# Kernel optimization log

Hardware: AMD Instinct MI355X
Metric: run time of the kernel (lower is better)

## Reference

```python
import jax, jax.numpy as jnp
import numpy as np

B_SZ, S, D_IN, D_OUT = 4, 4096, 4096, 4096
E, R = 16, 16


def setup_inputs() -> dict:
    key = jax.random.key(0)
    ks = jax.random.split(key, 6)
    x = jax.random.normal(ks[0], (B_SZ, S, D_IN), dtype=jnp.float32)
    W = jax.random.normal(ks[1], (D_OUT, D_IN), dtype=jnp.float32) * (1.0 / np.sqrt(D_IN))
    b = jax.random.normal(ks[2], (D_OUT,), dtype=jnp.float32) * 0.01
    A = jax.random.normal(ks[3], (E, R, D_IN), dtype=jnp.float32) * (1.0 / np.sqrt(D_IN))
    Bw = jax.random.normal(ks[4], (E, D_OUT, R), dtype=jnp.float32) * (1.0 / np.sqrt(R))
    probs = jax.random.uniform(ks[5], (E,), dtype=jnp.float32)
    probs = probs / jnp.sum(probs)  # router softmax-like cached probabilities
    return {"x": x, "W": W, "b": b, "A": A, "B": Bw, "probs": probs}


def reference(x, W, b, A, B, probs):
    # Base layer: out = x @ W^T + b  -> [b, s, d_out]
    out = jnp.einsum('bsd,od->bso', x, W) + b
    # LoRA mixture: sum_e probs[e] * (x @ A_e^T) @ B_e^T
    # h: [b, s, e, r] -- tiny (rank 16), then project up and weight by probs.
    h = jnp.einsum('bsd,erd->bser', x, A)
    contrib = jnp.einsum('bser,e,eor->bso', h, probs, B)
    return out + contrib
```

## Files before the change

kernel.cpp:

```cpp
#include <hip/hip_runtime.h>
#include <hip/hip_bf16.h>

typedef __bf16 bf16_t;
typedef __attribute__((ext_vector_type(8))) __bf16 bf16x8;
typedef __attribute__((ext_vector_type(4))) __bf16 bf16x4;
typedef __attribute__((ext_vector_type(4))) float f32x4;

#define GM 16384
#define GN 4096
#define GK 4096

#define GLOAD16(gp, lp)                                                        \
  __builtin_amdgcn_global_load_lds(                                            \
      (const __attribute__((address_space(1))) unsigned int*)(gp),             \
      (__attribute__((address_space(3))) unsigned int*)(lp), 16, 0, 0)

__global__ __launch_bounds__(256) void cvt_x_kernel(
    const float* __restrict__ in, bf16_t* __restrict__ outb) {
  long i = (long)blockIdx.x * blockDim.x + threadIdx.x;
  const f32x4* v = (const f32x4*)in;
  f32x4 a = v[4 * i + 0];
  f32x4 b = v[4 * i + 1];
  f32x4 c = v[4 * i + 2];
  f32x4 d = v[4 * i + 3];
  bf16x8 r0, r1;
  r0[0] = (__bf16)a[0]; r0[1] = (__bf16)a[1]; r0[2] = (__bf16)a[2]; r0[3] = (__bf16)a[3];
  r0[4] = (__bf16)b[0]; r0[5] = (__bf16)b[1]; r0[6] = (__bf16)b[2]; r0[7] = (__bf16)b[3];
  r1[0] = (__bf16)c[0]; r1[1] = (__bf16)c[1]; r1[2] = (__bf16)c[2]; r1[3] = (__bf16)c[3];
  r1[4] = (__bf16)d[0]; r1[5] = (__bf16)d[1]; r1[6] = (__bf16)d[2]; r1[7] = (__bf16)d[3];
  ((bf16x8*)outb)[2 * i + 0] = r0;
  ((bf16x8*)outb)[2 * i + 1] = r1;
}

__global__ __launch_bounds__(256) void make_bpt_kernel(
    const float* __restrict__ Bw, const float* __restrict__ probs,
    float* __restrict__ bpt) {
  int e = blockIdx.x >> 4;
  int o = ((blockIdx.x & 15) << 8) + threadIdx.x;
  float p = probs[e];
  const f32x4* src = (const f32x4*)(Bw + ((size_t)e << 16) + (size_t)o * 16);
  f32x4 v0 = src[0], v1 = src[1], v2 = src[2], v3 = src[3];
  float* dst = bpt + ((size_t)e * 16) * 4096 + o;
#pragma unroll
  for (int r = 0; r < 4; ++r) dst[r * 4096] = p * v0[r];
#pragma unroll
  for (int r = 0; r < 4; ++r) dst[(r + 4) * 4096] = p * v1[r];
#pragma unroll
  for (int r = 0; r < 4; ++r) dst[(r + 8) * 4096] = p * v2[r];
#pragma unroll
  for (int r = 0; r < 4; ++r) dst[(r + 12) * 4096] = p * v3[r];
}

__global__ __launch_bounds__(256) void weff_kernel(
    const float* __restrict__ W, const float* __restrict__ Aw,
    const float* __restrict__ bpt, bf16_t* __restrict__ weffp) {
  __shared__ __align__(16) float At[64 * 64];
  __shared__ __align__(16) float Bt[64 * 128];
  int tid = threadIdx.x;
  int d0 = (blockIdx.x & 63) << 6;
  int o0 = (blockIdx.x >> 6) << 7;
  int tx = tid & 7, ty = tid >> 3;

  float acc[4][8] = {};

  for (int kc = 0; kc < 256; kc += 64) {
    __syncthreads();
#pragma unroll
    for (int q = 0; q < 4; ++q) {
      int er = (tid >> 4) + q * 16;
      *(f32x4*)&At[er * 64 + (tid & 15) * 4] =
          *(const f32x4*)&Aw[(size_t)(kc + er) * 4096 + d0 + (tid & 15) * 4];
    }
#pragma unroll
    for (int q = 0; q < 8; ++q) {
      int er = (tid >> 5) + q * 8;
      *(f32x4*)&Bt[er * 128 + (tid & 31) * 4] =
          *(const f32x4*)&bpt[(size_t)(kc + er) * 4096 + o0 + (tid & 31) * 4];
    }
    __syncthreads();
#pragma unroll 4
    for (int kk = 0; kk < 64; ++kk) {
      f32x4 a0 = *(const f32x4*)&At[kk * 64 + tx * 8];
      f32x4 a1 = *(const f32x4*)&At[kk * 64 + tx * 8 + 4];
      f32x4 bv = *(const f32x4*)&Bt[kk * 128 + ty * 4];
#pragma unroll
      for (int i = 0; i < 4; ++i) {
#pragma unroll
        for (int j = 0; j < 4; ++j) {
          acc[i][j] = fmaf(bv[i], a0[j], acc[i][j]);
          acc[i][j + 4] = fmaf(bv[i], a1[j], acc[i][j + 4]);
        }
      }
    }
  }

#pragma unroll
  for (int i = 0; i < 4; ++i) {
    int o = o0 + ty * 4 + i;
    f32x4 w0 = *(const f32x4*)&W[(size_t)o * 4096 + d0 + tx * 8];
    f32x4 w1 = *(const f32x4*)&W[(size_t)o * 4096 + d0 + tx * 8 + 4];
    bf16x8 ov;
#pragma unroll
    for (int j = 0; j < 4; ++j) {
      ov[j] = (__bf16)(w0[j] + acc[i][j]);
      ov[j + 4] = (__bf16)(w1[j] + acc[i][j + 4]);
    }
    *(bf16x8*)&weffp[(size_t)o * 4096 + d0 + tx * 8] = ov;
  }
}

__global__ __launch_bounds__(256) void gemm_bt_bias_kernel(
    const bf16_t* __restrict__ xb, const bf16_t* __restrict__ weff,
    const float* __restrict__ bias, float* __restrict__ out) {
  __shared__ __align__(16) bf16_t As[2 * 128 * 32];
  __shared__ __align__(16) bf16_t Bs[2 * 128 * 32];

  int nwg = gridDim.x;
  int cpx = nwg >> 3;
  int bid = blockIdx.x;
  int swz = (bid & 7) * cpx + (bid >> 3);
  int mt = swz >> 5;
  int nt = swz & 31;
  int blkM = mt << 7;
  int blkN = nt << 7;

  int tid = threadIdx.x;
  int lane = tid & 63;
  int wv = tid >> 6;
  int wr = wv >> 1, wc = wv & 1;

  int srow = wv * 32 + (lane >> 2);
  int schunk = (lane & 3) ^ ((lane >> 3) & 3);
  const bf16_t* gA = xb + (long)(blkM + srow) * GK + schunk * 8;
  const bf16_t* gB = weff + (long)(blkN + srow) * GK + schunk * 8;
  int ldsOffA0 = (wv * 32) * 32;
  int ldsOffA1 = (wv * 32 + 16) * 32;

  int r_l = lane & 15;
  int pcidx = (lane >> 4) ^ ((lane >> 1) & 3);

  f32x4 acc[4][4];
#pragma unroll
  for (int i = 0; i < 4; ++i)
#pragma unroll
    for (int j = 0; j < 4; ++j) acc[i][j] = (f32x4){0.f, 0.f, 0.f, 0.f};

  GLOAD16(gA, As + ldsOffA0);
  GLOAD16(gA + 16 * GK, As + ldsOffA1);
  GLOAD16(gB, Bs + ldsOffA0);
  GLOAD16(gB + 16 * GK, Bs + ldsOffA1);
  __syncthreads();

  int cur = 0;
#define NT (GK / 32)
  for (int t = 0; t < NT; ++t) {
    if (t + 1 < NT) {
      int kn = (t + 1) * 32;
      int nb = (cur ^ 1) * 4096;
      GLOAD16(gA + kn, As + nb + ldsOffA0);
      GLOAD16(gA + kn + 16 * GK, As + nb + ldsOffA1);
      GLOAD16(gB + kn, Bs + nb + ldsOffA0);
      GLOAD16(gB + kn + 16 * GK, Bs + nb + ldsOffA1);
      __builtin_amdgcn_sched_barrier(0);
    }

    const bf16x8* AsV = (const bf16x8*)(As + cur * 4096);
    const bf16x8* BsV = (const bf16x8*)(Bs + cur * 4096);
    bf16x8 af[4], bfr[4];
#pragma unroll
    for (int mi = 0; mi < 4; ++mi)
      af[mi] = AsV[(wr * 64 + mi * 16 + r_l) * 4 + pcidx];
#pragma unroll
    for (int ni = 0; ni < 4; ++ni)
      bfr[ni] = BsV[(wc * 64 + ni * 16 + r_l) * 4 + pcidx];

#pragma unroll
    for (int mi = 0; mi < 4; ++mi)
#pragma unroll
      for (int ni = 0; ni < 4; ++ni)
        acc[mi][ni] = __builtin_amdgcn_mfma_f32_16x16x32_bf16(
            af[mi], bfr[ni], acc[mi][ni], 0, 0, 0);

    __syncthreads();
    cur ^= 1;
  }
#undef NT

  int n0 = blkN + wc * 64 + (lane & 15);
  int m0 = blkM + wr * 64 + ((lane >> 4) << 2);
#pragma unroll
  for (int ni = 0; ni < 4; ++ni) {
    float bv = bias[n0 + ni * 16];
#pragma unroll
    for (int mi = 0; mi < 4; ++mi) {
#pragma unroll
      for (int r = 0; r < 4; ++r) {
        out[(long)(m0 + mi * 16 + r) * GN + (n0 + ni * 16)] =
            acc[mi][ni][r] + bv;
      }
    }
  }
}

extern "C" void kernel_launch(void* const* d_in, const int* in_sizes, int n_in,
                              void* d_out, int out_size, void* d_ws,
                              size_t ws_size, hipStream_t stream) {
  const float* x = (const float*)d_in[0];
  const float* W = (const float*)d_in[1];
  const float* b = (const float*)d_in[2];
  const float* A = (const float*)d_in[3];
  const float* Bw = (const float*)d_in[4];
  const float* probs = (const float*)d_in[5];
  float* out = (float*)d_out;

  size_t need = (size_t)GM * GK * 2 + (size_t)GN * GK * 2 + 256ull * GN * 4;
  if (ws_size < need) return;

  bf16_t* xb = (bf16_t*)d_ws;
  bf16_t* weff = xb + (size_t)GM * GK;
  float* bpt = (float*)(weff + (size_t)GN * GK);

  cvt_x_kernel<<<16384, 256, 0, stream>>>(x, xb);
  make_bpt_kernel<<<256, 256, 0, stream>>>(Bw, probs, bpt);
  weff_kernel<<<2048, 256, 0, stream>>>(W, A, bpt, weff);
  gemm_bt_bias_kernel<<<4096, 256, 0, stream>>>(xb, weff, b, out);
}
```

Before: 1.267 ms.

## Enlarge GEMM tile to 256x256 with 8 waves and triple-buffered LDS pipeline

The main bf16 GEMM moves from 128x128 tiles with 4 waves and double buffering to 256x256 tiles with 8 waves. Each wave computes 128x64, LDS is triple-buffered, and explicit vmcnt waits keep two stages of loads in flight. The goal is more data reuse per byte loaded and better hiding of global-load latency. The weff kernel also shrinks its tile to 64x64 with twice the blocks. The cost is higher register pressure (32 accumulators per wave) and more LDS, which may limit occupancy.

Result: no change. 1.280 ms (+1.1%).

```diff
diff --git a/kernel.cpp b/kernel.cpp
--- a/kernel.cpp
+++ b/kernel.cpp
@@ -55,148 +55,148 @@
     const float* __restrict__ W, const float* __restrict__ Aw,
     const float* __restrict__ bpt, bf16_t* __restrict__ weffp) {
   __shared__ __align__(16) float At[64 * 64];
-  __shared__ __align__(16) float Bt[64 * 128];
+  __shared__ __align__(16) float Bt[64 * 64];
   int tid = threadIdx.x;
   int d0 = (blockIdx.x & 63) << 6;
-  int o0 = (blockIdx.x >> 6) << 7;
-  int tx = tid & 7, ty = tid >> 3;
-
-  float acc[4][8] = {};
+  int o0 = (blockIdx.x >> 6) << 6;
+  int tx = tid & 15, ty = tid >> 4;
+
+  float acc[4][4] = {};
 
   for (int kc = 0; kc < 256; kc += 64) {
     __syncthreads();
 #pragma unroll
     for (int q = 0; q < 4; ++q) {
-      int er = (tid >> 4) + q * 16;
-      *(f32x4*)&At[er * 64 + (tid & 15) * 4] =
-          *(const f32x4*)&Aw[(size_t)(kc + er) * 4096 + d0 + (tid & 15) * 4];
-    }
-#pragma unroll
-    for (int q = 0; q < 8; ++q) {
-      int er = (tid >> 5) + q * 8;
-      *(f32x4*)&Bt[er * 128 + (tid & 31) * 4] =
-          *(const f32x4*)&bpt[(size_t)(kc + er) * 4096 + o0 + (tid & 31) * 4];
+      int er_l = (tid >> 4) + q * 16;
+      f32x4 va = *(const f32x4*)&Aw[(long)(kc + er_l) * 4096 + d0 + tx * 4];
+      *(f32x4*)&At[er_l * 64 + tx * 4] = va;
+      f32x4 vb = *(const f32x4*)&bpt[(long)(kc + er_l) * 4096 + o0 + tx * 4];
+      *(f32x4*)&Bt[er_l * 64 + tx * 4] = vb;
     }
     __syncthreads();
-#pragma unroll 4
+#pragma unroll 8
     for (int kk = 0; kk < 64; ++kk) {
-      f32x4 a0 = *(const f32x4*)&At[kk * 64 + tx * 8];
-      f32x4 a1 = *(const f32x4*)&At[kk * 64 + tx * 8 + 4];
-      f32x4 bv = *(const f32x4*)&Bt[kk * 128 + ty * 4];
-#pragma unroll
-      for (int i = 0; i < 4; ++i) {
-#pragma unroll
-        for (int j = 0; j < 4; ++j) {
-          acc[i][j] = fmaf(bv[i], a0[j], acc[i][j]);
-          acc[i][j + 4] = fmaf(bv[i], a1[j], acc[i][j + 4]);
-        }
-      }
+      f32x4 av = *(const f32x4*)&At[kk * 64 + tx * 4];
+      f32x4 bv = *(const f32x4*)&Bt[kk * 64 + ty * 4];
+#pragma unroll
+      for (int i = 0; i < 4; ++i)
+#pragma unroll
+        for (int j = 0; j < 4; ++j) acc[i][j] = fmaf(bv[i], av[j], acc[i][j]);
     }
   }
 
 #pragma unroll
   for (int i = 0; i < 4; ++i) {
     int o = o0 + ty * 4 + i;
-    f32x4 w0 = *(const f32x4*)&W[(size_t)o * 4096 + d0 + tx * 8];
-    f32x4 w1 = *(const f32x4*)&W[(size_t)o * 4096 + d0 + tx * 8 + 4];
-    bf16x8 ov;
-#pragma unroll
-    for (int j = 0; j < 4; ++j) {
-      ov[j] = (__bf16)(w0[j] + acc[i][j]);
-      ov[j + 4] = (__bf16)(w1[j] + acc[i][j + 4]);
-    }
-    *(bf16x8*)&weffp[(size_t)o * 4096 + d0 + tx * 8] = ov;
-  }
-}
-
-__global__ __launch_bounds__(256) void gemm_bt_bias_kernel(
+    f32x4 w = *(const f32x4*)&W[(long)o * 4096 + d0 + tx * 4];
+    bf16x4 ov;
+#pragma unroll
+    for (int j = 0; j < 4; ++j) ov[j] = (__bf16)(w[j] + acc[i][j]);
+    *(bf16x4*)&weffp[(long)o * 4096 + d0 + tx * 4] = ov;
+  }
+}
+
+__global__ __launch_bounds__(512, 2) void gemm_bt_bias_kernel(
     const bf16_t* __restrict__ xb, const bf16_t* __restrict__ weff,
     const float* __restrict__ bias, float* __restrict__ out) {
-  __shared__ __align__(16) bf16_t As[2 * 128 * 32];
-  __shared__ __align__(16) bf16_t Bs[2 * 128 * 32];
+  __shared__ __align__(16) bf16_t AsL[3 * 256 * 32];
+  __shared__ __align__(16) bf16_t BsL[3 * 256 * 32];
 
   int nwg = gridDim.x;
   int cpx = nwg >> 3;
   int bid = blockIdx.x;
   int swz = (bid & 7) * cpx + (bid >> 3);
-  int mt = swz >> 5;
-  int nt = swz & 31;
-  int blkM = mt << 7;
-  int blkN = nt << 7;
+  int mt = swz >> 4;
+  int nt = swz & 15;
+  long blkM = (long)mt << 8;
+  long blkN = (long)nt << 8;
 
   int tid = threadIdx.x;
   int lane = tid & 63;
   int wv = tid >> 6;
-  int wr = wv >> 1, wc = wv & 1;
-
-  int srow = wv * 32 + (lane >> 2);
+  int wr = wv >> 2, wc = wv & 3;
+
+  int srow = wv * 16 + (lane >> 2);
   int schunk = (lane & 3) ^ ((lane >> 3) & 3);
-  const bf16_t* gA = xb + (long)(blkM + srow) * GK + schunk * 8;
-  const bf16_t* gB = weff + (long)(blkN + srow) * GK + schunk * 8;
-  int ldsOffA0 = (wv * 32) * 32;
-  int ldsOffA1 = (wv * 32 + 16) * 32;
+  const bf16_t* gA = xb + (blkM + srow) * GK + (long)schunk * 8;
+  const bf16_t* gB = weff + (blkN + srow) * GK + (long)schunk * 8;
+  int ldsOff0 = (wv * 16) * 32;
+  int ldsOff1 = (128 + wv * 16) * 32;
 
   int r_l = lane & 15;
   int pcidx = (lane >> 4) ^ ((lane >> 1) & 3);
 
-  f32x4 acc[4][4];
-#pragma unroll
-  for (int i = 0; i < 4; ++i)
+  f32x4 acc[8][4];
+#pragma unroll
+  for (int i = 0; i < 8; ++i)
 #pragma unroll
     for (int j = 0; j < 4; ++j) acc[i][j] = (f32x4){0.f, 0.f, 0.f, 0.f};
 
-  GLOAD16(gA, As + ldsOffA0);
-  GLOAD16(gA + 16 * GK, As + ldsOffA1);
-  GLOAD16(gB, Bs + ldsOffA0);
-  GLOAD16(gB + 16 * GK, Bs + ldsOffA1);
-  __syncthreads();
-
+#define STAGE(slot, kt)                                                        \
+  {                                                                            \
+    long ko = (long)(kt) * 32;                                                 \
+    bf16_t* la = AsL + (slot) * 8192;                                          \
+    bf16_t* lb = BsL + (slot) * 8192;                                          \
+    GLOAD16(gA + ko, la + ldsOff0);                                            \
+    GLOAD16(gA + ko + 128L * GK, la + ldsOff1);                                \
+    GLOAD16(gB + ko, lb + ldsOff0);                                            \
+    GLOAD16(gB + ko + 128L * GK, lb + ldsOff1);                                \
+  }
+
+  STAGE(0, 0);
+  STAGE(1, 1);
+
+  const int NTT = GK / 32;
   int cur = 0;
-#define NT (GK / 32)
-  for (int t = 0; t < NT; ++t) {
-    if (t + 1 < NT) {
-      int kn = (t + 1) * 32;
-      int nb = (cur ^ 1) * 4096;
-      GLOAD16(gA + kn, As + nb + ldsOffA0);
-      GLOAD16(gA + kn + 16 * GK, As + nb + ldsOffA1);
-      GLOAD16(gB + kn, Bs + nb + ldsOffA0);
-      GLOAD16(gB + kn + 16 * GK, Bs + nb + ldsOffA1);
-      __builtin_amdgcn_sched_barrier(0);
-    }
-
-    const bf16x8* AsV = (const bf16x8*)(As + cur * 4096);
-    const bf16x8* BsV = (const bf16x8*)(Bs + cur * 4096);
-    bf16x8 af[4], bfr[4];
-#pragma unroll
-    for (int mi = 0; mi < 4; ++mi)
-      af[mi] = AsV[(wr * 64 + mi * 16 + r_l) * 4 + pcidx];
+  for (int t = 0; t < NTT; ++t) {
+    int s2 = cur - 1; if (s2 < 0) s2 = 2;
+    if (t + 2 < NTT) STAGE(s2, t + 2);
+
+    if (t + 2 < NTT) {
+      asm volatile("s_waitcnt vmcnt(8)" ::: "memory");
+    } else if (t + 1 < NTT) {
+      asm volatile("s_waitcnt vmcnt(4)" ::: "memory");
+    } else {
+      asm volatile("s_waitcnt vmcnt(0)" ::: "memory");
+    }
+    __builtin_amdgcn_sched_barrier(0);
+    __builtin_amdgcn_s_barrier();
+    __builtin_amdgcn_sched_barrier(0);
+
+    const bf16x8* AsV = (const bf16x8*)(AsL + cur * 8192);
+    const bf16x8* BsV = (const bf16x8*)(BsL + cur * 8192);
+    bf16x8 af[8], bfr[4];
+#pragma unroll
+    for (int mi = 0; mi < 8; ++mi)
+      af[mi] = AsV[(wr * 128 + mi * 16 + r_l) * 4 + pcidx];
 #pragma unroll
     for (int ni = 0; ni < 4; ++ni)
       bfr[ni] = BsV[(wc * 64 + ni * 16 + r_l) * 4 + pcidx];
 
 #pragma unroll
-    for (int mi = 0; mi < 4; ++mi)
+    for (int mi = 0; mi < 8; ++mi)
 #pragma unroll
       for (int ni = 0; ni < 4; ++ni)
         acc[mi][ni] = __builtin_amdgcn_mfma_f32_16x16x32_bf16(
             af[mi], bfr[ni], acc[mi][ni], 0, 0, 0);
 
-    __syncthreads();
-    cur ^= 1;
-  }
-#undef NT
-
-  int n0 = blkN + wc * 64 + (lane & 15);
-  int m0 = blkM + wr * 64 + ((lane >> 4) << 2);
+    asm volatile("s_waitcnt lgkmcnt(0)" ::: "memory");
+    __builtin_amdgcn_sched_barrier(0);
+    __builtin_amdgcn_s_barrier();
+    cur = (cur + 1 == 3) ? 0 : cur + 1;
+  }
+#undef STAGE
+
+  long n0 = blkN + wc * 64 + (lane & 15);
+  long m0 = blkM + wr * 128 + ((lane >> 4) << 2);
 #pragma unroll
   for (int ni = 0; ni < 4; ++ni) {
     float bv = bias[n0 + ni * 16];
 #pragma unroll
-    for (int mi = 0; mi < 4; ++mi) {
+    for (int mi = 0; mi < 8; ++mi) {
 #pragma unroll
       for (int r = 0; r < 4; ++r) {
-        out[(long)(m0 + mi * 16 + r) * GN + (n0 + ni * 16)] =
-            acc[mi][ni][r] + bv;
+        out[(m0 + mi * 16 + r) * GN + (n0 + ni * 16)] = acc[mi][ni][r] + bv;
       }
     }
   }
@@ -222,6 +222,6 @@
 
   cvt_x_kernel<<<16384, 256, 0, stream>>>(x, xb);
   make_bpt_kernel<<<256, 256, 0, stream>>>(Bw, probs, bpt);
-  weff_kernel<<<2048, 256, 0, stream>>>(W, A, bpt, weff);
-  gemm_bt_bias_kernel<<<4096, 256, 0, stream>>>(xb, weff, b, out);
-}
+  weff_kernel<<<4096, 256, 0, stream>>>(W, A, bpt, weff);
+  gemm_bt_bias_kernel<<<1024, 512, 0, stream>>>(xb, weff, b, out);
+}
```
